# Kernel tuning notes

Hardware: AMD Instinct MI355X
Metric: run time of the kernel (lower is better)

The kernel has to match this reference:

```python
import jax, jax.numpy as jnp
import numpy as np


def setup_inputs() -> dict:
    key = jax.random.key(0)
    k1, k2 = jax.random.split(key)
    B, S, D, O = 4, 4096, 2048, 2048
    inputs = jax.random.normal(k1, (B, S, D), dtype=jnp.float32)
    # truncated-normal-like init with stddev 1/sqrt(fan_in)
    w = jax.random.normal(k2, (D, O), dtype=jnp.float32) * (1.0 / np.sqrt(D))
    b = jnp.zeros((O,), dtype=jnp.float32)
    return {"inputs": inputs, "w": w, "b": b}


def reference(inputs, w, b):
    # logsumexp-semiring linear layer (basis=None path):
    #   out = log(exp(inputs - max_in) @ exp(w - max_w)) + max_in + max_w + b
    max_inputs = jnp.max(inputs)          # global scalar max for stabilization
    max_w = jnp.max(w)
    exp_inputs = jnp.exp(inputs - max_inputs)   # [B, S, D]
    exp_w = jnp.exp(w - max_w)                  # [D, O]
    out = jnp.log(jnp.dot(exp_inputs, exp_w))   # [B, S, O]
    out = out + (max_inputs + max_w)
    out = out + b                               # broadcast bias over [B, S, O]
    return out
```

## Files before the change

kernel.cpp:

```cpp
#include <hip/hip_runtime.h>

typedef int   i32x4v __attribute__((ext_vector_type(4)));
typedef int   i32x8v __attribute__((ext_vector_type(8)));
typedef float f32x16 __attribute__((ext_vector_type(16)));

#define GLOBAL_AS(p) ((const __attribute__((address_space(1))) void*)(p))
#define LDS_AS(p)    ((__attribute__((address_space(3))) void*)(p))
#define BAR()     __builtin_amdgcn_s_barrier()
#define VMCNT(n)  asm volatile("s_waitcnt vmcnt(" #n ")" ::: "memory")

__device__ inline int fp4_code(float v) {
  return (v > 0.25f) + (v > 0.75f) + (v > 1.25f) + (v > 1.75f) +
         (v > 2.5f) + (v > 3.5f) + (v > 5.0f);
}

__global__ void expcvt_a4_kernel(const float* __restrict__ x,
                                 unsigned char* __restrict__ A4,
                                 unsigned char* __restrict__ SAt,
                                 int M, int K) {
  const int NKB = K >> 5;
  const int t = blockIdx.x * blockDim.x + threadIdx.x;
  const int m = t / NKB, kb = t - m * NKB;
  if (m >= M) return;
  const float4* xs4 = (const float4*)(x + (size_t)m * K + kb * 32);
  float a[32];
  float bm = -3.0e38f;
#pragma unroll
  for (int j = 0; j < 8; ++j) {
    float4 v = xs4[j];
    a[4 * j] = v.x; a[4 * j + 1] = v.y; a[4 * j + 2] = v.z; a[4 * j + 3] = v.w;
    bm = fmaxf(bm, fmaxf(fmaxf(v.x, v.y), fmaxf(v.z, v.w)));
  }
  int e = (int)ceilf(bm * 1.44269504f - 2.58496250f);
  e = min(127, max(-126, e));
  SAt[(size_t)kb * M + ((m >> 7) << 7) + ((m & 31) << 2) + ((m >> 5) & 3)] =
      (unsigned char)(e + 127);
  uint4 u;
  unsigned d[4];
#pragma unroll
  for (int g = 0; g < 4; ++g) {
    unsigned acc = 0;
#pragma unroll
    for (int j = 0; j < 8; ++j) {
      float v = exp2f(a[g * 8 + j] * 1.44269504f - (float)e);
      acc |= (unsigned)fp4_code(v) << (4 * j);
    }
    d[g] = acc;
  }
  u.x = d[0]; u.y = d[1]; u.z = d[2]; u.w = d[3];
  *(uint4*)(A4 + (size_t)m * (K >> 1) + kb * 16) = u;
}

__global__ void expcvt_wt4_kernel(const float* __restrict__ w,
                                  unsigned char* __restrict__ Bt4,
                                  unsigned char* __restrict__ SBt,
                                  int D, int O) {
  __shared__ float tile[32][33];
  int c0 = blockIdx.x * 32;
  int r0 = blockIdx.y * 32;
  int tx = threadIdx.x;
  int ty = threadIdx.y;
#pragma unroll
  for (int j = 0; j < 4; ++j) {
    int r = r0 + ty + j * 8;
    tile[ty + j * 8][tx] = __expf(w[(size_t)r * O + c0 + tx]);
  }
  __syncthreads();
  if (ty == 0) {
    const int n = c0 + tx;
    float bm = 0.0f;
#pragma unroll
    for (int d = 0; d < 32; ++d) bm = fmaxf(bm, tile[d][tx]);
    int e = (int)ceilf(__log2f(bm) - 2.58496250f);
    e = min(127, max(-126, e));
    SBt[(size_t)(r0 >> 5) * O + ((n >> 8) << 8) + ((n & 31) << 3) +
        ((n >> 5) & 7)] = (unsigned char)(e + 127);
    const float inv = exp2f(-(float)e);
    uint4 u;
    unsigned d4[4];
#pragma unroll
    for (int g = 0; g < 4; ++g) {
      unsigned acc = 0;
#pragma unroll
      for (int j = 0; j < 8; ++j)
        acc |= (unsigned)fp4_code(tile[g * 8 + j][tx] * inv) << (4 * j);
      d4[g] = acc;
    }
    u.x = d4[0]; u.y = d4[1]; u.z = d4[2]; u.w = d4[3];
    *(uint4*)(Bt4 + (size_t)n * (D >> 1) + (r0 >> 1)) = u;
  }
}


#define MFMA4(MB, NB, AV, BV, SAv, SBv)                                      \
  acc[MB][NB] = __builtin_amdgcn_mfma_scale_f32_32x32x64_f8f6f4(             \
      AV, BV, acc[MB][NB], 4, 4, 0, SAv, 0, SBv);

__global__ __launch_bounds__(256, 2) void gemm_mx4b_kernel(
    const unsigned char* __restrict__ A4, const unsigned char* __restrict__ Bt4,
    const unsigned char* __restrict__ SAt, const unsigned char* __restrict__ SBt,
    const float* __restrict__ bias, float* __restrict__ out,
    int M, int N, int K) {
  __shared__ char lds[79872];

  const int tid = threadIdx.x;
  const int wid = tid >> 6, lane = tid & 63;
  const int l31 = lane & 31, lk = lane >> 5;
  const int NTK = K >> 7;
  const size_t Kb = (size_t)K >> 1;

  const int cpx = gridDim.x >> 3;
  const int v   = (blockIdx.x & 7) * cpx + (blockIdx.x >> 3);
  const int nbn = N >> 8;
  const int bm  = v / nbn, bn = v % nbn;
  const int brow = bm << 7, bcol = bn << 8;

  const int swz = ((l31 & 6) << 3) ^ (l31 & 16);
  const int cR0 = (lk << 5) ^ swz;

  const char* gA[2];
  const char* gB[4];
#pragma unroll
  for (int i = 0; i < 2; ++i) {
    const int o = i * 4096 + tid * 16, row = o >> 6;
    const int sg = (((row & 6) << 3) ^ (row & 16)) >> 4;
    const int gl = ((o >> 4) & 3) ^ sg;
    const int gs = ((gl & 1) << 1) | (gl >> 1);
    gA[i] = (const char*)A4 + (size_t)(brow + row) * Kb + (gs << 4) + (o & 15);
  }
#pragma unroll
  for (int i = 0; i < 4; ++i) {
    const int o = i * 4096 + tid * 16, row = o >> 6;
    const int sg = (((row & 6) << 3) ^ (row & 16)) >> 4;
    const int gl = ((o >> 4) & 3) ^ sg;
    const int gs = ((gl & 1) << 1) | (gl >> 1);
    gB[i] = (const char*)Bt4 + (size_t)(bcol + row) * Kb + (gs << 4) + (o & 15);
  }
  const char* gSA = (const char*)SAt + (size_t)lk * M + brow + l31 * 4;
  const char* gSB = (const char*)SBt + bcol + (lane >> 1) * 8 + (lane & 1) * 4;

  auto STAGE = [&](int t, char* base) {
    const int tt = (t < NTK) ? t : NTK - 1;
    const int koff = tt << 6;
#pragma unroll
    for (int i = 0; i < 2; ++i)
      __builtin_amdgcn_global_load_lds(GLOBAL_AS(gA[i] + koff),
          LDS_AS(base + i * 4096 + wid * 1024), 16, 0, 0);
#pragma unroll
    for (int i = 0; i < 4; ++i)
      __builtin_amdgcn_global_load_lds(GLOBAL_AS(gB[i] + koff),
          LDS_AS(base + 8192 + i * 4096 + wid * 1024), 16, 0, 0);
    const size_t t4 = (size_t)(tt << 2);
    if (wid == 0) {
      __builtin_amdgcn_global_load_lds(GLOBAL_AS(gSA + t4 * M),
          LDS_AS(base + 24576), 4, 0, 0);
      __builtin_amdgcn_global_load_lds(GLOBAL_AS(gSA + t4 * M),
          LDS_AS(base + 26112), 4, 0, 0);
    } else if (wid == 1) {
      __builtin_amdgcn_global_load_lds(GLOBAL_AS(gSA + (t4 + 2) * M),
          LDS_AS(base + 24832), 4, 0, 0);
      __builtin_amdgcn_global_load_lds(GLOBAL_AS(gSA + (t4 + 2) * M),
          LDS_AS(base + 26368), 4, 0, 0);
    } else if (wid == 2) {
      __builtin_amdgcn_global_load_lds(GLOBAL_AS(gSB + t4 * N),
          LDS_AS(base + 25088), 4, 0, 0);
      __builtin_amdgcn_global_load_lds(GLOBAL_AS(gSB + (t4 + 1) * N),
          LDS_AS(base + 25344), 4, 0, 0);
    } else {
      __builtin_amdgcn_global_load_lds(GLOBAL_AS(gSB + (t4 + 2) * N),
          LDS_AS(base + 25600), 4, 0, 0);
      __builtin_amdgcn_global_load_lds(GLOBAL_AS(gSB + (t4 + 3) * N),
          LDS_AS(base + 25856), 4, 0, 0);
    }
  };

  f32x16 acc[4][2];
#pragma unroll
  for (int m = 0; m < 4; ++m)
#pragma unroll
    for (int n = 0; n < 2; ++n) acc[m][n] = (f32x16)0.0f;

  char* L0 = lds;
  char* L1 = lds + 26624;
  char* L2 = lds + 53248;

  STAGE(0, L0);
  STAGE(1, L1);
  VMCNT(8);
  BAR();

  const int shB = (wid & 1) << 4;

  for (int t = 0; t < NTK; ++t) {
    STAGE(t + 2, L2);

    const char* bA = L0;
    const char* bB = L0 + 8192;
#pragma unroll
    for (int h = 0; h < 2; ++h) {
      const int ch = cR0 ^ (h << 4);
      i32x8v a8[4], b8[2];
#pragma unroll
      for (int mb = 0; mb < 4; ++mb) {
        i32x4v f = *(const i32x4v*)(bA + (mb * 32 + l31) * 64 + ch);
        a8[mb] = __builtin_shufflevector(f, f, 0, 1, 2, 3, -1, -1, -1, -1);
      }
#pragma unroll
      for (int nb = 0; nb < 2; ++nb) {
        i32x4v f = *(const i32x4v*)(bB + (wid * 64 + nb * 32 + l31) * 64 + ch);
        b8[nb] = __builtin_shufflevector(f, f, 0, 1, 2, 3, -1, -1, -1, -1);
      }
      const int kb2 = 2 * h + lk;
      const int sAw = *(const int*)(L0 + 24576 + (kb2 * 32 + l31) * 4);
      const int2 sBd = *(const int2*)(L0 + 25088 + kb2 * 256 + l31 * 8);
      const int sel = (wid < 2) ? sBd.x : sBd.y;
      const int sB0 = (sel >> shB) & 0xFF;
      const int sB1 = (sel >> (shB + 8)) & 0xFF;
      const int sA0 = sAw & 0xFF, sA1 = (sAw >> 8) & 0xFF;
      const int sA2 = (sAw >> 16) & 0xFF, sA3 = (sAw >> 24) & 0xFF;
      MFMA4(0, 0, a8[0], b8[0], sA0, sB0) MFMA4(1, 0, a8[1], b8[0], sA1, sB0)
      MFMA4(2, 0, a8[2], b8[0], sA2, sB0) MFMA4(3, 0, a8[3], b8[0], sA3, sB0)
      MFMA4(0, 1, a8[0], b8[1], sA0, sB1) MFMA4(1, 1, a8[1], b8[1], sA1, sB1)
      MFMA4(2, 1, a8[2], b8[1], sA2, sB1) MFMA4(3, 1, a8[3], b8[1], sA3, sB1)
    }

    VMCNT(8);
    BAR();
    char* sw = L0; L0 = L1; L1 = L2; L2 = sw;
  }

  VMCNT(0);

  const int col0 = bcol + wid * 64 + l31;
  const int row0 = brow + lk * 4;
  const float bv0 = bias[col0], bv1 = bias[col0 + 32];
#pragma unroll
  for (int mb = 0; mb < 4; ++mb) {
#pragma unroll
    for (int rg = 0; rg < 16; ++rg) {
      const int row = row0 + mb * 32 + (rg & 3) + 8 * (rg >> 2);
      const size_t ro = (size_t)row * N + col0;
      __builtin_nontemporal_store(__logf(acc[mb][0][rg]) + bv0, &out[ro]);
      __builtin_nontemporal_store(__logf(acc[mb][1][rg]) + bv1, &out[ro + 32]);
    }
  }
}

extern "C" void kernel_launch(void* const* d_in, const int* in_sizes, int n_in,
                              void* d_out, int out_size, void* d_ws, size_t ws_size,
                              hipStream_t stream) {
  const float* inputs = (const float*)d_in[0];
  const float* w      = (const float*)d_in[1];
  const float* bias   = (const float*)d_in[2];
  float* out = (float*)d_out;

  const int O = in_sizes[2];
  const int D = in_sizes[1] / O;
  const size_t MD = (size_t)in_sizes[0];
  const int M = (int)(MD / (size_t)D);

  unsigned char* ws  = (unsigned char*)d_ws;
  unsigned char* A4  = ws;
  unsigned char* Bt4 = ws + MD / 2;
  unsigned char* SAt = Bt4 + (size_t)O * D / 2;
  unsigned char* SBt = SAt + MD / 32;

  const int nthr = (int)((MD / 32 + 255) / 256);
  expcvt_a4_kernel<<<nthr, 256, 0, stream>>>(inputs, A4, SAt, M, D);

  dim3 tg(O / 32, D / 32);
  expcvt_wt4_kernel<<<tg, dim3(32, 8), 0, stream>>>(w, Bt4, SBt, D, O);

  dim3 grid((M / 128) * (O / 256));
  gemm_mx4b_kernel<<<grid, 256, 0, stream>>>(A4, Bt4, SAt, SBt, bias, out,
                                             M, O, D);
}
```

Measured before the change: 103.5 us.

## Shrink GEMM block tile to 128x128 with 2x2 warp grid for higher occupancy

Reduces the block tile of the MXFP4 GEMM from 128x256 to 128x128 and arranges the four warps as a 2x2 grid of 64x64 subtiles. The B scale layout is repacked into 128-column groups so each warp loads scale data with a single uniform lds-direct load instead of per-warp branches. LDS drops to about 51KB and launch bounds rise to 3 blocks per CU, aiming at more latency hiding and better load balance. The cost is lower arithmetic intensity per block, so global and LDS traffic per FLOP goes up.

```diff
diff --git a/kernel.cpp b/kernel.cpp
--- a/kernel.cpp
+++ b/kernel.cpp
@@ -73,8 +73,8 @@
     for (int d = 0; d < 32; ++d) bm = fmaxf(bm, tile[d][tx]);
     int e = (int)ceilf(__log2f(bm) - 2.58496250f);
     e = min(127, max(-126, e));
-    SBt[(size_t)(r0 >> 5) * O + ((n >> 8) << 8) + ((n & 31) << 3) +
-        ((n >> 5) & 7)] = (unsigned char)(e + 127);
+    SBt[(size_t)(r0 >> 5) * O + ((n >> 7) << 7) + ((n & 31) << 2) +
+        ((n >> 5) & 3)] = (unsigned char)(e + 127);
     const float inv = exp2f(-(float)e);
     uint4 u;
     unsigned d4[4];
@@ -96,146 +96,123 @@
   acc[MB][NB] = __builtin_amdgcn_mfma_scale_f32_32x32x64_f8f6f4(             \
       AV, BV, acc[MB][NB], 4, 4, 0, SAv, 0, SBv);
 
-__global__ __launch_bounds__(256, 2) void gemm_mx4b_kernel(
+__global__ __launch_bounds__(256, 3) void gemm_mx4c_kernel(
     const unsigned char* __restrict__ A4, const unsigned char* __restrict__ Bt4,
     const unsigned char* __restrict__ SAt, const unsigned char* __restrict__ SBt,
     const float* __restrict__ bias, float* __restrict__ out,
     int M, int N, int K) {
-  __shared__ char lds[79872];
+  __shared__ char lds[52224];
 
   const int tid = threadIdx.x;
   const int wid = tid >> 6, lane = tid & 63;
+  const int wr = wid >> 1, wc = wid & 1;
   const int l31 = lane & 31, lk = lane >> 5;
   const int NTK = K >> 7;
   const size_t Kb = (size_t)K >> 1;
 
   const int cpx = gridDim.x >> 3;
   const int v   = (blockIdx.x & 7) * cpx + (blockIdx.x >> 3);
-  const int nbn = N >> 8;
+  const int nbn = N >> 7;
   const int bm  = v / nbn, bn = v % nbn;
-  const int brow = bm << 7, bcol = bn << 8;
+  const int brow = bm << 7, bcol = bn << 7;
 
   const int swz = ((l31 & 6) << 3) ^ (l31 & 16);
   const int cR0 = (lk << 5) ^ swz;
 
   const char* gA[2];
-  const char* gB[4];
+  const char* gB[2];
 #pragma unroll
   for (int i = 0; i < 2; ++i) {
     const int o = i * 4096 + tid * 16, row = o >> 6;
     const int sg = (((row & 6) << 3) ^ (row & 16)) >> 4;
     const int gl = ((o >> 4) & 3) ^ sg;
     const int gs = ((gl & 1) << 1) | (gl >> 1);
-    gA[i] = (const char*)A4 + (size_t)(brow + row) * Kb + (gs << 4) + (o & 15);
-  }
-#pragma unroll
-  for (int i = 0; i < 4; ++i) {
-    const int o = i * 4096 + tid * 16, row = o >> 6;
-    const int sg = (((row & 6) << 3) ^ (row & 16)) >> 4;
-    const int gl = ((o >> 4) & 3) ^ sg;
-    const int gs = ((gl & 1) << 1) | (gl >> 1);
-    gB[i] = (const char*)Bt4 + (size_t)(bcol + row) * Kb + (gs << 4) + (o & 15);
-  }
-  const char* gSA = (const char*)SAt + (size_t)lk * M + brow + l31 * 4;
-  const char* gSB = (const char*)SBt + bcol + (lane >> 1) * 8 + (lane & 1) * 4;
+    gA[i] = (const char*)A4 + (size_t)(brow + row) * Kb + (gs << 4);
+    gB[i] = (const char*)Bt4 + (size_t)(bcol + row) * Kb + (gs << 4);
+  }
+  const char* gS;
+  size_t sstep;
+  if (wid < 2) {
+    gS = (const char*)SAt + ((size_t)(lane >> 5) + 2 * wid) * M + brow + l31 * 4;
+    sstep = 4 * (size_t)M;
+  } else {
+    gS = (const char*)SBt + ((size_t)(lane >> 5) + 2 * (wid - 2)) * N + bcol +
+         l31 * 4;
+    sstep = 4 * (size_t)N;
+  }
 
   auto STAGE = [&](int t, char* base) {
     const int tt = (t < NTK) ? t : NTK - 1;
     const int koff = tt << 6;
 #pragma unroll
-    for (int i = 0; i < 2; ++i)
+    for (int i = 0; i < 2; ++i) {
       __builtin_amdgcn_global_load_lds(GLOBAL_AS(gA[i] + koff),
           LDS_AS(base + i * 4096 + wid * 1024), 16, 0, 0);
-#pragma unroll
-    for (int i = 0; i < 4; ++i)
       __builtin_amdgcn_global_load_lds(GLOBAL_AS(gB[i] + koff),
           LDS_AS(base + 8192 + i * 4096 + wid * 1024), 16, 0, 0);
-    const size_t t4 = (size_t)(tt << 2);
-    if (wid == 0) {
-      __builtin_amdgcn_global_load_lds(GLOBAL_AS(gSA + t4 * M),
-          LDS_AS(base + 24576), 4, 0, 0);
-      __builtin_amdgcn_global_load_lds(GLOBAL_AS(gSA + t4 * M),
-          LDS_AS(base + 26112), 4, 0, 0);
-    } else if (wid == 1) {
-      __builtin_amdgcn_global_load_lds(GLOBAL_AS(gSA + (t4 + 2) * M),
-          LDS_AS(base + 24832), 4, 0, 0);
-      __builtin_amdgcn_global_load_lds(GLOBAL_AS(gSA + (t4 + 2) * M),
-          LDS_AS(base + 26368), 4, 0, 0);
-    } else if (wid == 2) {
-      __builtin_amdgcn_global_load_lds(GLOBAL_AS(gSB + t4 * N),
-          LDS_AS(base + 25088), 4, 0, 0);
-      __builtin_amdgcn_global_load_lds(GLOBAL_AS(gSB + (t4 + 1) * N),
-          LDS_AS(base + 25344), 4, 0, 0);
-    } else {
-      __builtin_amdgcn_global_load_lds(GLOBAL_AS(gSB + (t4 + 2) * N),
-          LDS_AS(base + 25600), 4, 0, 0);
-      __builtin_amdgcn_global_load_lds(GLOBAL_AS(gSB + (t4 + 3) * N),
-          LDS_AS(base + 25856), 4, 0, 0);
-    }
+    }
+    __builtin_amdgcn_global_load_lds(GLOBAL_AS(gS + (size_t)tt * sstep),
+        LDS_AS(base + 16384 + wid * 256 + lane * 4), 4, 0, 0);
   };
 
-  f32x16 acc[4][2];
-#pragma unroll
-  for (int m = 0; m < 4; ++m)
+  f32x16 acc[2][2];
+#pragma unroll
+  for (int m = 0; m < 2; ++m)
 #pragma unroll
     for (int n = 0; n < 2; ++n) acc[m][n] = (f32x16)0.0f;
 
   char* L0 = lds;
-  char* L1 = lds + 26624;
-  char* L2 = lds + 53248;
+  char* L1 = lds + 17408;
+  char* L2 = lds + 34816;
 
   STAGE(0, L0);
   STAGE(1, L1);
-  VMCNT(8);
+  VMCNT(5);
   BAR();
 
-  const int shB = (wid & 1) << 4;
+  const int shA = wr << 4;
+  const int shB = wc << 4;
 
   for (int t = 0; t < NTK; ++t) {
     STAGE(t + 2, L2);
 
-    const char* bA = L0;
-    const char* bB = L0 + 8192;
+    const char* bA = L0 + wr * 4096;
+    const char* bB = L0 + 8192 + wc * 4096;
 #pragma unroll
     for (int h = 0; h < 2; ++h) {
       const int ch = cR0 ^ (h << 4);
-      i32x8v a8[4], b8[2];
-#pragma unroll
-      for (int mb = 0; mb < 4; ++mb) {
+      i32x8v a8[2], b8[2];
+#pragma unroll
+      for (int mb = 0; mb < 2; ++mb) {
         i32x4v f = *(const i32x4v*)(bA + (mb * 32 + l31) * 64 + ch);
         a8[mb] = __builtin_shufflevector(f, f, 0, 1, 2, 3, -1, -1, -1, -1);
       }
 #pragma unroll
       for (int nb = 0; nb < 2; ++nb) {
-        i32x4v f = *(const i32x4v*)(bB + (wid * 64 + nb * 32 + l31) * 64 + ch);
+        i32x4v f = *(const i32x4v*)(bB + (nb * 32 + l31) * 64 + ch);
         b8[nb] = __builtin_shufflevector(f, f, 0, 1, 2, 3, -1, -1, -1, -1);
       }
       const int kb2 = 2 * h + lk;
-      const int sAw = *(const int*)(L0 + 24576 + (kb2 * 32 + l31) * 4);
-      const int2 sBd = *(const int2*)(L0 + 25088 + kb2 * 256 + l31 * 8);
-      const int sel = (wid < 2) ? sBd.x : sBd.y;
-      const int sB0 = (sel >> shB) & 0xFF;
-      const int sB1 = (sel >> (shB + 8)) & 0xFF;
-      const int sA0 = sAw & 0xFF, sA1 = (sAw >> 8) & 0xFF;
-      const int sA2 = (sAw >> 16) & 0xFF, sA3 = (sAw >> 24) & 0xFF;
-      MFMA4(0, 0, a8[0], b8[0], sA0, sB0) MFMA4(1, 0, a8[1], b8[0], sA1, sB0)
-      MFMA4(2, 0, a8[2], b8[0], sA2, sB0) MFMA4(3, 0, a8[3], b8[0], sA3, sB0)
-      MFMA4(0, 1, a8[0], b8[1], sA0, sB1) MFMA4(1, 1, a8[1], b8[1], sA1, sB1)
-      MFMA4(2, 1, a8[2], b8[1], sA2, sB1) MFMA4(3, 1, a8[3], b8[1], sA3, sB1)
-    }
-
-    VMCNT(8);
+      const int saw = *(const int*)(L0 + 16384 + kb2 * 128 + l31 * 4);
+      const int sbw = *(const int*)(L0 + 16896 + kb2 * 128 + l31 * 4);
+      const int sA0 = (saw >> shA) & 0xFF, sA1 = (saw >> (shA + 8)) & 0xFF;
+      const int sB0 = (sbw >> shB) & 0xFF, sB1 = (sbw >> (shB + 8)) & 0xFF;
+      MFMA4(0, 0, a8[0], b8[0], sA0, sB0)
+      MFMA4(1, 0, a8[1], b8[0], sA1, sB0)
+      MFMA4(0, 1, a8[0], b8[1], sA0, sB1)
+      MFMA4(1, 1, a8[1], b8[1], sA1, sB1)
+    }
+
+    VMCNT(5);
     BAR();
     char* sw = L0; L0 = L1; L1 = L2; L2 = sw;
   }
 
-  VMCNT(0);
-
-  const int col0 = bcol + wid * 64 + l31;
-  const int row0 = brow + lk * 4;
+  const int col0 = bcol + wc * 64 + l31;
+  const int row0 = brow + wr * 64 + lk * 4;
   const float bv0 = bias[col0], bv1 = bias[col0 + 32];
 #pragma unroll
-  for (int mb = 0; mb < 4; ++mb) {
+  for (int mb = 0; mb < 2; ++mb) {
 #pragma unroll
     for (int rg = 0; rg < 16; ++rg) {
       const int row = row0 + mb * 32 + (rg & 3) + 8 * (rg >> 2);
@@ -271,7 +248,7 @@
   dim3 tg(O / 32, D / 32);
   expcvt_wt4_kernel<<<tg, dim3(32, 8), 0, stream>>>(w, Bt4, SBt, D, O);
 
-  dim3 grid((M / 128) * (O / 256));
-  gemm_mx4b_kernel<<<grid, 256, 0, stream>>>(A4, Bt4, SAt, SBt, bias, out,
+  dim3 grid((M / 128) * (O / 128));
+  gemm_mx4c_kernel<<<grid, 256, 0, stream>>>(A4, Bt4, SAt, SBt, bias, out,
                                              M, O, D);
 }
```

Result: faster. 90.47 us (-12.6%).
